# Performance work log

Hardware: AMD Instinct MI355X
Metric: run time of the kernel (lower is better)

Reference implementation:

```python
import jax, jax.numpy as jnp
import numpy as np
from jax import lax

B, T, I, H = 8192, 512, 3, 25  # batch, seq_len, input_size, hidden_size


def setup_inputs() -> dict:
    key = jax.random.key(0)
    ks = jax.random.split(key, 4)
    x = jax.random.normal(ks[0], (B, T, I), dtype=jnp.float32)
    # xavier-uniform-ish scale for w_ih, orthogonal-ish (plain normal here) for w_hh
    w_ih = jax.random.normal(ks[1], (4 * H, I), dtype=jnp.float32) * 0.5
    w_hh = jax.random.normal(ks[2], (4 * H, H), dtype=jnp.float32) * 0.2
    b_ih = jnp.zeros((4 * H,), dtype=jnp.float32)
    # PyTorch init in module: forget-gate bias (second quarter) set to 1 on each bias
    b_ih = b_ih.at[H:2 * H].set(1.0)
    b_hh = jnp.zeros((4 * H,), dtype=jnp.float32)
    b_hh = b_hh.at[H:2 * H].set(1.0)
    w_lin = jax.random.normal(ks[3], (1, H), dtype=jnp.float32) * 0.3
    b_lin = jnp.zeros((1,), dtype=jnp.float32)
    return {"x": x, "w_ih": w_ih, "w_hh": w_hh, "b_ih": b_ih, "b_hh": b_hh,
            "w_lin": w_lin, "b_lin": b_lin}


def _lstm_last_h(x, w_ih, w_hh, b_ih, b_hh):
    # x: [B, T, I]; returns final hidden state h_T: [B, H]
    b = b_ih + b_hh  # [4H]
    xT = jnp.swapaxes(x, 0, 1)  # [T, B, I]

    def step(carry, x_t):
        h, c = carry
        gates = x_t @ w_ih.T + h @ w_hh.T + b  # [B, 4H]
        i, f, g, o = jnp.split(gates, 4, axis=-1)  # PyTorch gate order i,f,g,o
        i = jax.nn.sigmoid(i)
        f = jax.nn.sigmoid(f)
        g = jnp.tanh(g)
        o = jax.nn.sigmoid(o)
        c = f * c + i * g
        h = o * jnp.tanh(c)
        return (h, c), None

    h0 = jnp.zeros((x.shape[0], w_hh.shape[1]), dtype=x.dtype)
    (h, _), _ = lax.scan(step, (h0, h0), xT)
    return h


def reference(x, w_ih, w_hh, b_ih, b_hh, w_lin, b_lin):
    h_last = _lstm_last_h(x, w_ih, w_hh, b_ih, b_hh)  # [B, H]
    return h_last @ w_lin.T + b_lin  # [B, 1]
```

## Files before the change

### kernel.cpp

```cpp
#include <hip/hip_runtime.h>
#include <hip/hip_bf16.h>


#define TSTEPS 512
#define ISZ 3
#define HSZ 25
#define NTILES 512
#define TSTRIDE 40

typedef __attribute__((ext_vector_type(8))) short bf16x8;
typedef __attribute__((ext_vector_type(4))) float f32x4;

__device__ __forceinline__ unsigned short bf16_bits(float v) {
    return __builtin_bit_cast(unsigned short, __float2bfloat16(v));
}
__device__ __forceinline__ unsigned int pack_bf16(float lo, float hi) {
    return ((unsigned int)bf16_bits(hi) << 16) | (unsigned int)bf16_bits(lo);
}

__device__ __forceinline__ void lstm_act(const f32x4 acc, float& c, float& h) {
    const float K1 = 1.442695040888963f;
    const float K2 = 2.885390081777927f;
    const float e0 = __builtin_amdgcn_exp2f(-K1 * acc[0]);
    const float e1 = __builtin_amdgcn_exp2f(-K1 * acc[1]);
    const float e2 = __builtin_amdgcn_exp2f(fminf(-K2 * acc[2], 126.0f));
    const float e3 = __builtin_amdgcn_exp2f(-K1 * acc[3]);
    const float f  = __builtin_amdgcn_rcpf(1.0f + e1);
    const float ig = (1.0f - e2) * __builtin_amdgcn_rcpf((1.0f + e0) * (1.0f + e2));
    c = fmaf(f, c, ig);
    const float ec = __builtin_amdgcn_exp2f(fminf(-K2 * c, 126.0f));
    h = (1.0f - ec) * __builtin_amdgcn_rcpf((1.0f + e3) * (1.0f + ec));
}

__global__ __launch_bounds__(256) void lstm_mfma(
    const float* __restrict__ x,
    const float* __restrict__ w_ih,
    const float* __restrict__ w_hh,
    const float* __restrict__ b_ih,
    const float* __restrict__ b_hh,
    const float* __restrict__ w_lin,
    const float* __restrict__ b_lin,
    float* __restrict__ out)
{
    __shared__ uint2 xpk[TSTEPS * 16];
    __shared__ short hb[2][16 * TSTRIDE];
    __shared__ float outred[4][16];

    const int tid  = threadIdx.x;
    const int w    = tid >> 6;
    const int lane = tid & 63;
    const int n    = lane & 15;
    const int q    = lane >> 4;
    const bool isq0 = (q == 0);

    for (int i = tid; i < 2 * 16 * TSTRIDE; i += 256) ((short*)hb)[i] = 0;

    {
        const int bsel = tid >> 4, sub16 = tid & 15;
        const float* __restrict__ g = x + (size_t)(blockIdx.x * 16 + bsel) * (TSTEPS * ISZ);
        #pragma unroll
        for (int it = 0; it < 8; ++it) {
            const int tg = sub16 + 16 * it;
            const float4* f4 = (const float4*)(g + tg * 12);
            float4 a = f4[0], b4 = f4[1], c4 = f4[2];
            const float s[4][3] = { {a.x, a.y, a.z}, {a.w, b4.x, b4.y},
                                    {b4.z, b4.w, c4.x}, {c4.y, c4.z, c4.w} };
            #pragma unroll
            for (int u = 0; u < 4; ++u) {
                uint2 d;
                d.x = pack_bf16(s[u][0], s[u][1]);
                d.y = pack_bf16(s[u][2], 1.0f);
                xpk[(tg * 4 + u) * 16 + bsel] = d;
            }
        }
    }

    bf16x8 afrag[2];
    #pragma unroll
    for (int idx = 0; idx < 2; ++idx) {
        const int T = 2 * w + idx;
        #pragma unroll
        for (int j = 0; j < 8; ++j) {
            const int k = q * 8 + j;
            const int r = 16 * T + n;
            const int u = r >> 2, g = r & 3;
            float v = 0.0f;
            if (u < HSZ) {
                const int orow = g * HSZ + u;
                if (k < ISZ)            v = w_ih[orow * ISZ + k];
                else if (k == ISZ)      v = b_ih[orow] + b_hh[orow];
                else if (k < 4 + HSZ)   v = w_hh[orow * HSZ + (k - 4)];
            }
            afrag[idx][j] = (short)bf16_bits(v);
        }
    }

    __syncthreads();

    float c0 = 0.f, c1 = 0.f, h0 = 0.f, h1 = 0.f;

    #pragma unroll 1
    for (int t = 0; t < TSTEPS; ++t) {
        const short* __restrict__ rrow = &hb[t & 1][n * TSTRIDE];
        short* __restrict__ wrow = &hb[(t + 1) & 1][n * TSTRIDE];

        const uint2 xdw = xpk[t * 16 + n];
        bf16x8 bfrag = *reinterpret_cast<const bf16x8*>(rrow + q * 8);
        {
            uint4 bi = __builtin_bit_cast(uint4, bfrag);
            if (isq0) { bi.x = xdw.x; bi.y = xdw.y; }
            bfrag = __builtin_bit_cast(bf16x8, bi);
        }

        f32x4 acc0 = __builtin_amdgcn_mfma_f32_16x16x32_bf16(
            afrag[0], bfrag, (f32x4){0.f, 0.f, 0.f, 0.f}, 0, 0, 0);
        f32x4 acc1;
        if (w < 3)
            acc1 = __builtin_amdgcn_mfma_f32_16x16x32_bf16(
                afrag[1], bfrag, (f32x4){0.f, 0.f, 0.f, 0.f}, 0, 0, 0);

        lstm_act(acc0, c0, h0);
        if (w < 3 || isq0)
            wrow[4 + 8 * w + q] = (short)bf16_bits(h0);
        if (w < 3) {
            lstm_act(acc1, c1, h1);
            wrow[4 + 8 * w + 4 + q] = (short)bf16_bits(h1);
        }

        __syncthreads();
    }

    float v = 0.f;
    {
        const int u0 = 8 * w + q;
        if (u0 < HSZ) v = w_lin[u0] * h0;
        if (w < 3)    v = fmaf(w_lin[8 * w + 4 + q], h1, v);
    }
    v += __shfl_xor(v, 16);
    v += __shfl_xor(v, 32);
    if (lane < 16) outred[w][lane] = v;
    __syncthreads();
    if (tid < 16)
        out[blockIdx.x * 16 + tid] =
            outred[0][tid] + outred[1][tid] + outred[2][tid] + outred[3][tid] + b_lin[0];
}

extern "C" void kernel_launch(void* const* d_in, const int* in_sizes, int n_in,
                              void* d_out, int out_size, void* d_ws, size_t ws_size,
                              hipStream_t stream) {
    const float* x     = (const float*)d_in[0];
    const float* w_ih  = (const float*)d_in[1];
    const float* w_hh  = (const float*)d_in[2];
    const float* b_ih  = (const float*)d_in[3];
    const float* b_hh  = (const float*)d_in[4];
    const float* w_lin = (const float*)d_in[5];
    const float* b_lin = (const float*)d_in[6];
    float* out = (float*)d_out;

    lstm_mfma<<<NTILES, 256, 0, stream>>>(x, w_ih, w_hh, b_ih, b_hh,
                                          w_lin, b_lin, out);
}
```

Measured before the change: 303.0 us.

## Split gate tiles across seven wavefronts, one MFMA per wave per step

Each block now runs 7 wavefronts instead of 4. Each wave owns one 16-row gate tile, so it issues a single MFMA and one activation per timestep instead of two serial ones. This shortens the per-step critical path of the recurrence. The x value for the next step is also prefetched from LDS one iteration early. In exchange the per-step barrier spans more waves, and occupancy and register limits change because each block is larger.

New measurement: 301.6 us. No clear change (-0.5%).

```diff
diff --git a/kernel.cpp b/kernel.cpp
--- a/kernel.cpp
+++ b/kernel.cpp
@@ -6,6 +6,7 @@
 #define ISZ 3
 #define HSZ 25
 #define NTILES 512
+#define NW 7
 #define TSTRIDE 40
 
 typedef __attribute__((ext_vector_type(8))) short bf16x8;
@@ -32,7 +33,7 @@
     h = (1.0f - ec) * __builtin_amdgcn_rcpf((1.0f + e3) * (1.0f + ec));
 }
 
-__global__ __launch_bounds__(256) void lstm_mfma(
+__global__ __launch_bounds__(NW * 64) void lstm_mfma(
     const float* __restrict__ x,
     const float* __restrict__ w_ih,
     const float* __restrict__ w_hh,
@@ -44,7 +45,7 @@
 {
     __shared__ uint2 xpk[TSTEPS * 16];
     __shared__ short hb[2][16 * TSTRIDE];
-    __shared__ float outred[4][16];
+    __shared__ float outred[NW][16];
 
     const int tid  = threadIdx.x;
     const int w    = tid >> 6;
@@ -52,10 +53,11 @@
     const int n    = lane & 15;
     const int q    = lane >> 4;
     const bool isq0 = (q == 0);
+    const int u    = 4 * w + q;
 
-    for (int i = tid; i < 2 * 16 * TSTRIDE; i += 256) ((short*)hb)[i] = 0;
+    for (int i = tid; i < 2 * 16 * TSTRIDE; i += NW * 64) ((short*)hb)[i] = 0;
 
-    {
+    if (tid < 256) {
         const int bsel = tid >> 4, sub16 = tid & 15;
         const float* __restrict__ g = x + (size_t)(blockIdx.x * 16 + bsel) * (TSTEPS * ISZ);
         #pragma unroll
@@ -66,45 +68,44 @@
             const float s[4][3] = { {a.x, a.y, a.z}, {a.w, b4.x, b4.y},
                                     {b4.z, b4.w, c4.x}, {c4.y, c4.z, c4.w} };
             #pragma unroll
-            for (int u = 0; u < 4; ++u) {
+            for (int uu = 0; uu < 4; ++uu) {
                 uint2 d;
-                d.x = pack_bf16(s[u][0], s[u][1]);
-                d.y = pack_bf16(s[u][2], 1.0f);
-                xpk[(tg * 4 + u) * 16 + bsel] = d;
+                d.x = pack_bf16(s[uu][0], s[uu][1]);
+                d.y = pack_bf16(s[uu][2], 1.0f);
+                xpk[(tg * 4 + uu) * 16 + bsel] = d;
             }
         }
     }
 
-    bf16x8 afrag[2];
+    bf16x8 afrag;
     #pragma unroll
-    for (int idx = 0; idx < 2; ++idx) {
-        const int T = 2 * w + idx;
-        #pragma unroll
-        for (int j = 0; j < 8; ++j) {
-            const int k = q * 8 + j;
-            const int r = 16 * T + n;
-            const int u = r >> 2, g = r & 3;
-            float v = 0.0f;
-            if (u < HSZ) {
-                const int orow = g * HSZ + u;
-                if (k < ISZ)            v = w_ih[orow * ISZ + k];
-                else if (k == ISZ)      v = b_ih[orow] + b_hh[orow];
-                else if (k < 4 + HSZ)   v = w_hh[orow * HSZ + (k - 4)];
-            }
-            afrag[idx][j] = (short)bf16_bits(v);
+    for (int j = 0; j < 8; ++j) {
+        const int k = q * 8 + j;
+        const int r = 16 * w + n;
+        const int uu = r >> 2, g = r & 3;
+        float v = 0.0f;
+        if (uu < HSZ) {
+            const int orow = g * HSZ + uu;
+            if (k < ISZ)            v = w_ih[orow * ISZ + k];
+            else if (k == ISZ)      v = b_ih[orow] + b_hh[orow];
+            else if (k < 4 + HSZ)   v = w_hh[orow * HSZ + (k - 4)];
         }
+        afrag[j] = (short)bf16_bits(v);
     }
 
     __syncthreads();
 
-    float c0 = 0.f, c1 = 0.f, h0 = 0.f, h1 = 0.f;
+    float c = 0.f, h = 0.f;
+    uint2 xdw = xpk[n];
 
     #pragma unroll 1
     for (int t = 0; t < TSTEPS; ++t) {
+        const int tn = (t + 1 < TSTEPS) ? t + 1 : t;
+        const uint2 xnxt = xpk[tn * 16 + n];
+
         const short* __restrict__ rrow = &hb[t & 1][n * TSTRIDE];
         short* __restrict__ wrow = &hb[(t + 1) & 1][n * TSTRIDE];
 
-        const uint2 xdw = xpk[t * 16 + n];
         bf16x8 bfrag = *reinterpret_cast<const bf16x8*>(rrow + q * 8);
         {
             uint4 bi = __builtin_bit_cast(uint4, bfrag);
@@ -112,37 +113,30 @@
             bfrag = __builtin_bit_cast(bf16x8, bi);
         }
 
-        f32x4 acc0 = __builtin_amdgcn_mfma_f32_16x16x32_bf16(
-            afrag[0], bfrag, (f32x4){0.f, 0.f, 0.f, 0.f}, 0, 0, 0);
-        f32x4 acc1;
-        if (w < 3)
-            acc1 = __builtin_amdgcn_mfma_f32_16x16x32_bf16(
-                afrag[1], bfrag, (f32x4){0.f, 0.f, 0.f, 0.f}, 0, 0, 0);
+        const f32x4 acc = __builtin_amdgcn_mfma_f32_16x16x32_bf16(
+            afrag, bfrag, (f32x4){0.f, 0.f, 0.f, 0.f}, 0, 0, 0);
 
-        lstm_act(acc0, c0, h0);
-        if (w < 3 || isq0)
-            wrow[4 + 8 * w + q] = (short)bf16_bits(h0);
-        if (w < 3) {
-            lstm_act(acc1, c1, h1);
-            wrow[4 + 8 * w + 4 + q] = (short)bf16_bits(h1);
-        }
+        lstm_act(acc, c, h);
 
+        if (w < 6 || isq0)
+            wrow[4 + u] = (short)bf16_bits(h);
+
+        xdw = xnxt;
         __syncthreads();
     }
 
     float v = 0.f;
-    {
-        const int u0 = 8 * w + q;
-        if (u0 < HSZ) v = w_lin[u0] * h0;
-        if (w < 3)    v = fmaf(w_lin[8 * w + 4 + q], h1, v);
-    }
+    if (w < 6 || isq0) v = w_lin[u] * h;
     v += __shfl_xor(v, 16);
     v += __shfl_xor(v, 32);
     if (lane < 16) outred[w][lane] = v;
     __syncthreads();
-    if (tid < 16)
-        out[blockIdx.x * 16 + tid] =
-            outred[0][tid] + outred[1][tid] + outred[2][tid] + outred[3][tid] + b_lin[0];
+    if (tid < 16) {
+        float s = b_lin[0];
+        #pragma unroll
+        for (int k = 0; k < NW; ++k) s += outred[k][tid];
+        out[blockIdx.x * 16 + tid] = s;
+    }
 }
 
 extern "C" void kernel_launch(void* const* d_in, const int* in_sizes, int n_in,
@@ -157,6 +151,6 @@
     const float* b_lin = (const float*)d_in[6];
     float* out = (float*)d_out;
 
-    lstm_mfma<<<NTILES, 256, 0, stream>>>(x, w_ih, w_hh, b_ih, b_hh,
-                                          w_lin, b_lin, out);
+    lstm_mfma<<<NTILES, NW * 64, 0, stream>>>(x, w_ih, w_hh, b_ih, b_hh,
+                                              w_lin, b_lin, out);
 }
```
